# Kernel optimization log

Hardware: AMD Instinct MI355X
Metric: run time of the kernel (lower is better)

Reference implementation:

```python
import jax, jax.numpy as jnp
import numpy as np

B, S, E, H, NL, V = 32, 512, 768, 1024, 5, 30522


def setup_inputs() -> dict:
    key = jax.random.key(0)
    k = jax.random.split(key, 12)
    s = 0.02
    return {
        "x": jax.random.randint(k[0], (B, S), 0, V),
        "emotion_mask": jax.random.randint(k[1], (V,), 0, 2) > 0,
        "all_hidden": jax.random.normal(k[2], (B, S, E), jnp.float32),
        "word_embedding_vocab": jax.random.normal(k[3], (V, E), jnp.float32),
        "Wih0": jax.random.normal(k[4], (4 * H, E), jnp.float32) * s,
        "Whh0": jax.random.normal(k[5], (4 * H, H), jnp.float32) * s,
        "bih0": jnp.zeros((4 * H,), jnp.float32),
        "bhh0": jnp.zeros((4 * H,), jnp.float32),
        "Wih1": jax.random.normal(k[6], (4 * H, H), jnp.float32) * s,
        "Whh1": jax.random.normal(k[7], (4 * H, H), jnp.float32) * s,
        "bih1": jnp.zeros((4 * H,), jnp.float32),
        "bhh1": jnp.zeros((4 * H,), jnp.float32),
        "W1": jax.random.normal(k[8], (100, H), jnp.float32) * s,
        "b1": jnp.zeros((100,), jnp.float32),
        "W2": jax.random.normal(k[9], (1, 100), jnp.float32) * s,
        "b2": jnp.zeros((1,), jnp.float32),
        "Wf": jax.random.normal(k[10], (NL, H), jnp.float32) * s,
        "bf": jnp.zeros((NL,), jnp.float32),
    }


def _lstm_layer(xs, Wih, Whh, bih, bhh):
    # xs: [B, S, D]; PyTorch gate order i, f, g, o
    Bm = xs.shape[0]
    Hm = Whh.shape[1]
    b = bih + bhh

    def step(carry, xt):
        h, c = carry
        g = xt @ Wih.T + h @ Whh.T + b
        i, f, gg, o = jnp.split(g, 4, axis=-1)
        c = jax.nn.sigmoid(f) * c + jax.nn.sigmoid(i) * jnp.tanh(gg)
        h = jax.nn.sigmoid(o) * jnp.tanh(c)
        return (h, c), h

    init = (jnp.zeros((Bm, Hm), xs.dtype), jnp.zeros((Bm, Hm), xs.dtype))
    (h, c), ys = jax.lax.scan(step, init, xs.transpose(1, 0, 2))
    return ys.transpose(1, 0, 2), h, c


def reference(x, emotion_mask, all_hidden, word_embedding_vocab,
              Wih0, Whh0, bih0, bhh0, Wih1, Whh1, bih1, bhh1,
              W1, b1, W2, b2, Wf, bf):
    # Fused replacement for the per-token python loop:
    # blend BERT hidden with vocab embedding where token is in emotion vocab
    # (positions index >= 1 only, as in the original loop range(1, len)).
    emo = emotion_mask[x]                                  # [B, S]
    pos_ok = jnp.arange(x.shape[1]) >= 1                   # [S]
    m = (emo & pos_ok[None, :])[..., None]                 # [B, S, 1]
    hdn = jnp.where(m, (word_embedding_vocab[x] + all_hidden) * 0.5, all_hidden)

    # 2-layer batch_first LSTM (eval mode -> dropout is identity)
    out1, _, _ = _lstm_layer(hdn, Wih0, Whh0, bih0, bhh0)
    out2, _, _ = _lstm_layer(out1, Wih1, Whh1, bih1, bhh1)

    # Structured self-attention
    a = jnp.tanh(out2 @ W1.T + b1)                         # [B, S, 100]
    a = a @ W2.T + b2                                      # [B, S, 1]
    w = jax.nn.softmax(a, axis=1)                          # softmax over seq
    sent = jnp.einsum('bsr,bsh->brh', w, out2)             # [B, 1, H]
    avg = jnp.sum(sent, axis=1)                            # r = 1
    logits = avg @ Wf.T + bf                               # [B, num_labels]
    return logits, w.squeeze(2)
```

## Files before the change

### kernel.cpp

```cpp
#include <hip/hip_runtime.h>

#define B_   32
#define S_   512
#define E_   768
#define H_   1024
#define G4_  4096
#define BS_  16384

__device__ __forceinline__ unsigned short f2b(float f) {
    union { float f; unsigned u; } a; a.f = f;
    unsigned r = a.u + 0x7FFFu + ((a.u >> 16) & 1u);
    return (unsigned short)(r >> 16);
}
__device__ __forceinline__ float b2f(unsigned short u) {
    union { unsigned u; float f; } a; a.u = ((unsigned)u) << 16;
    return a.f;
}

typedef __attribute__((ext_vector_type(8))) short bh8;
typedef __attribute__((ext_vector_type(4))) float f4x;

#define ALOAD(p)     __hip_atomic_load((p), __ATOMIC_RELAXED, __HIP_MEMORY_SCOPE_AGENT)
#define ASTORE(p, v) __hip_atomic_store((p), (v), __ATOMIC_RELAXED, __HIP_MEMORY_SCOPE_AGENT)

__global__ void detect_mask_k(const unsigned* __restrict__ m, unsigned* __restrict__ flag) {
    int t = threadIdx.x;
    unsigned bad = 0;
#pragma unroll
    for (int i = 0; i < 4; ++i) { unsigned v = m[t * 4 + i]; bad |= (v > 1u); }
    unsigned long long bb = __ballot(bad != 0u);
    if (t == 0) flag[0] = (bb != 0ull) ? 1u : 0u;
}

__global__ void blend_k(const int* __restrict__ x, const void* __restrict__ mask,
                        const float* __restrict__ hid, const float* __restrict__ emb,
                        const unsigned* __restrict__ flag, unsigned short* __restrict__ hdn) {
    int row = blockIdx.x;
    int t = threadIdx.x;
    if (t >= 192) return;
    int s = row & 511;
    int tok = x[row];
    bool emo;
    if (flag[0]) emo = ((const unsigned char*)mask)[tok] != 0;
    else         emo = ((const int*)mask)[tok] != 0;
    bool bl = emo && (s >= 1);
    float4 v = *(const float4*)(hid + (size_t)row * E_ + t * 4);
    if (bl) {
        float4 e = *(const float4*)(emb + (size_t)tok * E_ + t * 4);
        v.x = (v.x + e.x) * 0.5f; v.y = (v.y + e.y) * 0.5f;
        v.z = (v.z + e.z) * 0.5f; v.w = (v.w + e.w) * 0.5f;
    }
    ushort4 o; o.x = f2b(v.x); o.y = f2b(v.y); o.z = f2b(v.z); o.w = f2b(v.w);
    *(ushort4*)(hdn + (size_t)row * E_ + t * 4) = o;
}

__global__ void cvt_k(const float* __restrict__ in, unsigned short* __restrict__ o, int n) {
    int i = (blockIdx.x * blockDim.x + threadIdx.x) * 4;
    if (i >= n) return;
    float4 v = *(const float4*)(in + i);
    ushort4 u; u.x = f2b(v.x); u.y = f2b(v.y); u.z = f2b(v.z); u.w = f2b(v.w);
    *(ushort4*)(o + i) = u;
}

template <int AF32, int PERM>
__global__ __launch_bounds__(256) void gemm_k(const void* __restrict__ Ap,
        const unsigned short* __restrict__ Bp, unsigned short* __restrict__ Cp,
        int K, int Nreal, int ldc, const float* __restrict__ bias, int act) {
    __shared__ char smA[16384];
    __shared__ char smB[16384];
    const int tid = threadIdx.x, l = tid & 63, w = tid >> 6;
    const int m0 = blockIdx.x * 128, n0 = blockIdx.y * 128;
    const int wr = (w >> 1) * 64, wc = (w & 1) * 64;
    f4x acc[4][4] = {};
    for (int k0 = 0; k0 < K; k0 += 64) {
#pragma unroll
        for (int it = 0; it < 4; ++it) {
            int idx = it * 256 + tid;
            int row = idx >> 3, c16 = idx & 7;
            int sof = (row * 128 + c16 * 16) ^ ((row & 7) << 4);
            bh8 va;
            if (AF32) {
                const float* ap = (const float*)Ap + (size_t)(m0 + row) * K + k0 + c16 * 8;
                float4 f0 = *(const float4*)ap;
                float4 f1 = *(const float4*)(ap + 4);
                va[0] = (short)f2b(f0.x); va[1] = (short)f2b(f0.y);
                va[2] = (short)f2b(f0.z); va[3] = (short)f2b(f0.w);
                va[4] = (short)f2b(f1.x); va[5] = (short)f2b(f1.y);
                va[6] = (short)f2b(f1.z); va[7] = (short)f2b(f1.w);
            } else {
                va = *(const bh8*)((const unsigned short*)Ap + (size_t)(m0 + row) * K + k0 + c16 * 8);
            }
            *(bh8*)(smA + sof) = va;
            int nr = n0 + row;
            bh8 vb = {0, 0, 0, 0, 0, 0, 0, 0};
            if (nr < Nreal) vb = *(const bh8*)(Bp + (size_t)nr * K + k0 + c16 * 8);
            *(bh8*)(smB + sof) = vb;
        }
        __syncthreads();
#pragma unroll
        for (int kk = 0; kk < 2; ++kk) {
            bh8 af[4], bf8[4];
#pragma unroll
            for (int f = 0; f < 4; ++f) {
                int ra = wr + f * 16 + (l & 15);
                af[f] = *(const bh8*)(smA + ((ra * 128 + kk * 64 + ((l >> 4) << 4)) ^ ((ra & 7) << 4)));
                int rb = wc + f * 16 + (l & 15);
                bf8[f] = *(const bh8*)(smB + ((rb * 128 + kk * 64 + ((l >> 4) << 4)) ^ ((rb & 7) << 4)));
            }
#pragma unroll
            for (int fi = 0; fi < 4; ++fi)
#pragma unroll
                for (int fj = 0; fj < 4; ++fj)
                    acc[fi][fj] = __builtin_amdgcn_mfma_f32_16x16x32_bf16(af[fi], bf8[fj], acc[fi][fj], 0, 0, 0);
        }
        __syncthreads();
    }
#pragma unroll
    for (int fi = 0; fi < 4; ++fi) {
        int rb2 = wr + fi * 16 + ((l >> 4) << 2);
#pragma unroll
        for (int fj = 0; fj < 4; ++fj) {
            int cc = n0 + wc + fj * 16 + (l & 15);
            if (cc < Nreal) {
                float bv = bias ? bias[cc] : 0.f;
                int cw = cc;
                if (PERM) {
                    int gate = cc >> 10, rem = cc & 1023;
                    cw = (rem >> 3) * 32 + gate * 8 + (cc & 7);
                }
#pragma unroll
                for (int i = 0; i < 4; ++i) {
                    float xv = acc[fi][fj][i] + bv;
                    if (act) xv = tanhf(xv);
                    Cp[(size_t)(m0 + rb2 + i) * ldc + cw] = f2b(xv);
                }
            }
        }
    }
}

__global__ __launch_bounds__(256, 1) void recur2_k(
        const unsigned short* __restrict__ G,
        const unsigned short* __restrict__ Whh0,
        const float* __restrict__ bih0, const float* __restrict__ bhh0,
        const unsigned short* __restrict__ Wih1,
        const unsigned short* __restrict__ Whh1,
        const float* __restrict__ bih1, const float* __restrict__ bhh1,
        float* __restrict__ out2,
        unsigned* __restrict__ h0b, unsigned* __restrict__ h1b,
        unsigned* __restrict__ slots) {
    __shared__ __align__(16) char w_lds[131072];
    __shared__ float red_s[4][32][33];
    __shared__ float bias_s[32];
    unsigned short* g_s = (unsigned short*)(w_lds + 65536);

    const int tid = threadIdx.x, l = tid & 63, wv = tid >> 6, ln = l;
    const int wg = blockIdx.x, lay = wg >> 7, w = wg & 127;
    const int u0 = w * 8;
    const int q = l >> 4, r0 = l & 15;
    const int bb = tid >> 3, uu = tid & 7;

#pragma unroll
    for (int it = 0; it < 16; ++it) {
        int idx = it * 256 + tid;
        int r = idx >> 7, c16 = idx & 127;
        int Rg = (r >> 3) * 1024 + u0 + (r & 7);
        int dst = (r * 2048 + c16 * 16) ^ ((r & 7) << 4);
        if (lay == 0) {
            *(bh8*)(w_lds + dst) = *(const bh8*)(Whh0 + (size_t)Rg * 1024 + c16 * 8);
        } else {
            *(bh8*)(w_lds + dst) = *(const bh8*)(Wih1 + (size_t)Rg * 1024 + c16 * 8);
            *(bh8*)(w_lds + 65536 + dst) = *(const bh8*)(Whh1 + (size_t)Rg * 1024 + c16 * 8);
        }
    }
    if (tid < 32) {
        int Rg = (tid >> 3) * 1024 + u0 + (tid & 7);
        bias_s[tid] = (lay == 0) ? (bih0[Rg] + bhh0[Rg]) : (bih1[Rg] + bhh1[Rg]);
    }
    {
        unsigned* hb = (lay == 0) ? h0b : h1b;
        if (tid < 128) ASTORE(&hb[(size_t)w * 128 + tid], 0u);
    }
    float cS = 0.f;
    __syncthreads();
    if (tid == 0) ASTORE(&slots[wg], 1u);

    if (lay == 0) {
        const int gb = tid >> 2, gq = tid & 3;
        bh8 greg = {};
        if (tid < 128)
            greg = *(const bh8*)(G + (size_t)gb * 512 * G4_ + w * 32 + gq * 8);
        for (int g = 1; g <= 512; ++g) {
            int s = g - 1;
            for (;;) {
                unsigned s0v = ALOAD(&slots[ln]);
                unsigned s1v = ALOAD(&slots[64 + ln]);
                if (__all(s0v >= (unsigned)g && s1v >= (unsigned)g)) break;
                __builtin_amdgcn_s_sleep(2);
            }
            const char* hp = (const char*)h0b + (size_t)(g - 1) * 65536;
            f4x a00 = {}, a01 = {}, a10 = {}, a11 = {};
#pragma unroll
            for (int s8 = 0; s8 < 8; ++s8) {
                int k0 = wv * 256 + s8 * 32 + q * 8;
                int blk = k0 >> 3;
                bh8 x0 = *(const bh8*)(hp + blk * 512 + r0 * 16);
                bh8 x1 = *(const bh8*)(hp + blk * 512 + (16 + r0) * 16);
                bh8 w0 = *(const bh8*)(w_lds + ((r0 * 2048 + k0 * 2) ^ ((r0 & 7) << 4)));
                bh8 w1 = *(const bh8*)(w_lds + (((16 + r0) * 2048 + k0 * 2) ^ ((r0 & 7) << 4)));
                a00 = __builtin_amdgcn_mfma_f32_16x16x32_bf16(x0, w0, a00, 0, 0, 0);
                a01 = __builtin_amdgcn_mfma_f32_16x16x32_bf16(x0, w1, a01, 0, 0, 0);
                a10 = __builtin_amdgcn_mfma_f32_16x16x32_bf16(x1, w0, a10, 0, 0, 0);
                a11 = __builtin_amdgcn_mfma_f32_16x16x32_bf16(x1, w1, a11, 0, 0, 0);
            }
#pragma unroll
            for (int i = 0; i < 4; ++i) {
                int ro = q * 4 + i;
                red_s[wv][ro][r0]           = a00[i];
                red_s[wv][ro][16 + r0]      = a01[i];
                red_s[wv][16 + ro][r0]      = a10[i];
                red_s[wv][16 + ro][16 + r0] = a11[i];
            }
            if (tid < 128) {
                *(bh8*)(g_s + gb * 32 + gq * 8) = greg;
                int sn = (s + 1 < 512) ? s + 1 : s;
                greg = *(const bh8*)(G + ((size_t)gb * 512 + sn) * G4_ + w * 32 + gq * 8);
            }
            __syncthreads();
            float gv[4];
#pragma unroll
            for (int gg = 0; gg < 4; ++gg) {
                int rr = gg * 8 + uu;
                gv[gg] = red_s[0][bb][rr] + red_s[1][bb][rr] + red_s[2][bb][rr] + red_s[3][bb][rr]
                       + b2f(g_s[bb * 32 + rr]) + bias_s[rr];
            }
            float si = 1.f / (1.f + __expf(-gv[0]));
            float sf = 1.f / (1.f + __expf(-gv[1]));
            float so = 1.f / (1.f + __expf(-gv[3]));
            float cn = sf * cS + si * tanhf(gv[2]);
            float hv = so * tanhf(cn);
            cS = cn;
            unsigned hu = f2b(hv);
            unsigned nb = __shfl_down(hu, 1);
            if ((uu & 1) == 0)
                ASTORE(&h0b[(size_t)g * 16384 + w * 128 + bb * 4 + (uu >> 1)], hu | (nb << 16));
            __syncthreads();
            if (tid == 0) ASTORE(&slots[wg], (unsigned)(g + 1));
        }
    } else {
        for (int g = 2; g <= 513; ++g) {
            int s = g - 2;
            for (;;) {
                unsigned s0v = ALOAD(&slots[ln]);
                unsigned s1v = ALOAD(&slots[64 + ln]);
                unsigned s2v = ALOAD(&slots[128 + ln]);
                unsigned s3v = ALOAD(&slots[192 + ln]);
                if (__all(s0v >= (unsigned)g && s1v >= (unsigned)g &&
                          s2v >= (unsigned)(g - 1) && s3v >= (unsigned)(g - 1))) break;
                __builtin_amdgcn_s_sleep(2);
            }
            const char* hpA = (const char*)h0b + (size_t)(g - 1) * 65536;
            const char* hpB = (const char*)h1b + (size_t)(g - 2) * 65536;
            f4x a00 = {}, a01 = {}, a10 = {}, a11 = {};
#pragma unroll
            for (int s8 = 0; s8 < 8; ++s8) {
                int k0 = wv * 256 + s8 * 32 + q * 8;
                int blk = k0 >> 3;
                bh8 x0 = *(const bh8*)(hpA + blk * 512 + r0 * 16);
                bh8 x1 = *(const bh8*)(hpA + blk * 512 + (16 + r0) * 16);
                bh8 w0 = *(const bh8*)(w_lds + ((r0 * 2048 + k0 * 2) ^ ((r0 & 7) << 4)));
                bh8 w1 = *(const bh8*)(w_lds + (((16 + r0) * 2048 + k0 * 2) ^ ((r0 & 7) << 4)));
                a00 = __builtin_amdgcn_mfma_f32_16x16x32_bf16(x0, w0, a00, 0, 0, 0);
                a01 = __builtin_amdgcn_mfma_f32_16x16x32_bf16(x0, w1, a01, 0, 0, 0);
                a10 = __builtin_amdgcn_mfma_f32_16x16x32_bf16(x1, w0, a10, 0, 0, 0);
                a11 = __builtin_amdgcn_mfma_f32_16x16x32_bf16(x1, w1, a11, 0, 0, 0);
            }
#pragma unroll
            for (int s8 = 0; s8 < 8; ++s8) {
                int k0 = wv * 256 + s8 * 32 + q * 8;
                int blk = k0 >> 3;
                bh8 x0 = *(const bh8*)(hpB + blk * 512 + r0 * 16);
                bh8 x1 = *(const bh8*)(hpB + blk * 512 + (16 + r0) * 16);
                bh8 w0 = *(const bh8*)(w_lds + 65536 + ((r0 * 2048 + k0 * 2) ^ ((r0 & 7) << 4)));
                bh8 w1 = *(const bh8*)(w_lds + 65536 + (((16 + r0) * 2048 + k0 * 2) ^ ((r0 & 7) << 4)));
                a00 = __builtin_amdgcn_mfma_f32_16x16x32_bf16(x0, w0, a00, 0, 0, 0);
                a01 = __builtin_amdgcn_mfma_f32_16x16x32_bf16(x0, w1, a01, 0, 0, 0);
                a10 = __builtin_amdgcn_mfma_f32_16x16x32_bf16(x1, w0, a10, 0, 0, 0);
                a11 = __builtin_amdgcn_mfma_f32_16x16x32_bf16(x1, w1, a11, 0, 0, 0);
            }
#pragma unroll
            for (int i = 0; i < 4; ++i) {
                int ro = q * 4 + i;
                red_s[wv][ro][r0]           = a00[i];
                red_s[wv][ro][16 + r0]      = a01[i];
                red_s[wv][16 + ro][r0]      = a10[i];
                red_s[wv][16 + ro][16 + r0] = a11[i];
            }
            __syncthreads();
            float gv[4];
#pragma unroll
            for (int gg = 0; gg < 4; ++gg) {
                int rr = gg * 8 + uu;
                gv[gg] = red_s[0][bb][rr] + red_s[1][bb][rr] + red_s[2][bb][rr] + red_s[3][bb][rr]
                       + bias_s[rr];
            }
            float si = 1.f / (1.f + __expf(-gv[0]));
            float sf = 1.f / (1.f + __expf(-gv[1]));
            float so = 1.f / (1.f + __expf(-gv[3]));
            float cn = sf * cS + si * tanhf(gv[2]);
            float hv = so * tanhf(cn);
            cS = cn;
            unsigned hu = f2b(hv);
            unsigned nb = __shfl_down(hu, 1);
            if ((uu & 1) == 0)
                ASTORE(&h1b[(size_t)(g - 1) * 16384 + w * 128 + bb * 4 + (uu >> 1)], hu | (nb << 16));
            out2[((size_t)bb * 512 + s) * 1024 + u0 + uu] = hv;
            __syncthreads();
            if (tid == 0) ASTORE(&slots[wg], (unsigned)g);
        }
    }
}

__global__ void score_k(const unsigned short* __restrict__ a1, const float* __restrict__ W2,
                        float* __restrict__ sc) {
    int r = blockIdx.x * blockDim.x + threadIdx.x;
    const unsigned short* p = a1 + (size_t)r * 104;
    float s = 0.f;
#pragma unroll
    for (int i = 0; i < 100; ++i) s += b2f(p[i]) * W2[i];
    sc[r] = s;
}

__global__ __launch_bounds__(256) void attn_k(const float* __restrict__ sc,
        const float* __restrict__ out2, const float* __restrict__ Wf,
        const float* __restrict__ bf, float* __restrict__ out) {
    int b = blockIdx.x, t = threadIdx.x;
    __shared__ float p[512];
    __shared__ float red[256];
    __shared__ float sent[1024];
    float s0 = sc[b * 512 + t], s1 = sc[b * 512 + 256 + t];
    red[t] = fmaxf(s0, s1);
    __syncthreads();
    for (int o = 128; o > 0; o >>= 1) { if (t < o) red[t] = fmaxf(red[t], red[t + o]); __syncthreads(); }
    float M = red[0];
    __syncthreads();
    float e0 = __expf(s0 - M), e1 = __expf(s1 - M);
    red[t] = e0 + e1;
    __syncthreads();
    for (int o = 128; o > 0; o >>= 1) { if (t < o) red[t] += red[t + o]; __syncthreads(); }
    float inv = 1.f / red[0];
    float w0 = e0 * inv, w1 = e1 * inv;
    p[t] = w0; p[t + 256] = w1;
    out[160 + b * 512 + t] = w0;
    out[160 + b * 512 + 256 + t] = w1;
    __syncthreads();
    float4 acc = {0.f, 0.f, 0.f, 0.f};
    for (int s = 0; s < 512; ++s) {
        float ws = p[s];
        float4 v = *(const float4*)(out2 + ((size_t)b * 512 + s) * H_ + t * 4);
        acc.x += ws * v.x; acc.y += ws * v.y; acc.z += ws * v.z; acc.w += ws * v.w;
    }
    *(float4*)(sent + t * 4) = acc;
    __syncthreads();
    int wv = t >> 6, ln = t & 63;
    for (int n = wv; n < 5; n += 4) {
        float prt = 0.f;
        for (int k = ln; k < 1024; k += 64) prt += sent[k] * Wf[n * 1024 + k];
#pragma unroll
        for (int o = 32; o > 0; o >>= 1) prt += __shfl_down(prt, o);
        if (ln == 0) out[b * 5 + n] = prt + bf[n];
    }
}

#define OFF_SLOT  ((size_t)0)
#define OFF_FLAG  ((size_t)1024)
#define OFF_WH0   ((size_t)4096)
#define OFF_W1I   (OFF_WH0 + (size_t)G4_ * H_ * 2)
#define OFF_WH1   (OFF_W1I + (size_t)G4_ * H_ * 2)
#define OFF_W1A   (OFF_WH1 + (size_t)G4_ * H_ * 2)
#define OFF_G     (OFF_W1A + (size_t)262144)
#define OFF_OUT2  (OFF_G + (size_t)BS_ * G4_ * 2)
#define OFF_HDN   OFF_OUT2
#define OFF_W0    (OFF_HDN + (size_t)BS_ * E_ * 2)
#define OFF_A1    (OFF_OUT2 + (size_t)BS_ * H_ * 4)
#define OFF_SC    (OFF_A1 + (size_t)BS_ * 104 * 2)
#define OFF_H0    ((size_t)230293504)
#define OFF_H1    (OFF_H0 + (size_t)513 * 65536)

extern "C" void kernel_launch(void* const* d_in, const int* in_sizes, int n_in,
                              void* d_out, int out_size, void* d_ws, size_t ws_size,
                              hipStream_t stream) {
    const int*   x    = (const int*)d_in[0];
    const void*  mask = d_in[1];
    const float* hid  = (const float*)d_in[2];
    const float* emb  = (const float*)d_in[3];
    const float* Wih0 = (const float*)d_in[4];
    const float* Whh0 = (const float*)d_in[5];
    const float* bih0 = (const float*)d_in[6];
    const float* bhh0 = (const float*)d_in[7];
    const float* Wih1 = (const float*)d_in[8];
    const float* Whh1 = (const float*)d_in[9];
    const float* bih1 = (const float*)d_in[10];
    const float* bhh1 = (const float*)d_in[11];
    const float* W1   = (const float*)d_in[12];
    const float* b1   = (const float*)d_in[13];
    const float* W2   = (const float*)d_in[14];
    const float* Wf   = (const float*)d_in[16];
    const float* bfp  = (const float*)d_in[17];
    float* out = (float*)d_out;
    char* ws = (char*)d_ws;

    unsigned*       slots = (unsigned*)(ws + OFF_SLOT);
    unsigned*       flag  = (unsigned*)(ws + OFF_FLAG);
    unsigned short* wh0b  = (unsigned short*)(ws + OFF_WH0);
    unsigned short* w1ib  = (unsigned short*)(ws + OFF_W1I);
    unsigned short* wh1b  = (unsigned short*)(ws + OFF_WH1);
    unsigned short* w1ab  = (unsigned short*)(ws + OFF_W1A);
    unsigned short* Gb    = (unsigned short*)(ws + OFF_G);
    float*          out2f = (float*)(ws + OFF_OUT2);
    unsigned short* hdn   = (unsigned short*)(ws + OFF_HDN);
    unsigned short* w0b   = (unsigned short*)(ws + OFF_W0);
    unsigned short* a1b   = (unsigned short*)(ws + OFF_A1);
    float*          scb   = (float*)(ws + OFF_SC);
    unsigned*       h0b   = (unsigned*)(ws + OFF_H0);
    unsigned*       h1b   = (unsigned*)(ws + OFF_H1);

    hipMemsetAsync(ws, 0, 4096, stream);

    detect_mask_k<<<1, 64, 0, stream>>>((const unsigned*)mask, flag);
    blend_k<<<BS_, 192, 0, stream>>>(x, mask, hid, emb, flag, hdn);
    cvt_k<<<3072, 256, 0, stream>>>(Wih0, w0b, G4_ * E_);
    cvt_k<<<4096, 256, 0, stream>>>(Whh0, wh0b, G4_ * H_);
    cvt_k<<<4096, 256, 0, stream>>>(Wih1, w1ib, G4_ * H_);
    cvt_k<<<4096, 256, 0, stream>>>(Whh1, wh1b, G4_ * H_);
    cvt_k<<<100, 256, 0, stream>>>(W1, w1ab, 100 * H_);

    gemm_k<0, 1><<<dim3(BS_ / 128, G4_ / 128), 256, 0, stream>>>(hdn, w0b, Gb, E_, G4_, G4_, nullptr, 0);

    {
        const unsigned short* a0 = Gb;
        const unsigned short* a1p = wh0b;
        const float* a2 = bih0; const float* a3 = bhh0;
        const unsigned short* a4 = w1ib; const unsigned short* a5 = wh1b;
        const float* a6 = bih1; const float* a7 = bhh1;
        float* a8 = out2f; unsigned* a9 = h0b; unsigned* a10 = h1b; unsigned* a11 = slots;
        void* args[] = {&a0, &a1p, &a2, &a3, &a4, &a5, &a6, &a7, &a8, &a9, &a10, &a11};
        hipLaunchCooperativeKernel((const void*)recur2_k, dim3(256), dim3(256), args, 0, stream);
    }

    gemm_k<1, 0><<<dim3(BS_ / 128, 1), 256, 0, stream>>>(out2f, w1ab, a1b, H_, 100, 104, b1, 1);
    score_k<<<BS_ / 256, 256, 0, stream>>>(a1b, W2, scb);
    attn_k<<<B_, 256, 0, stream>>>(scb, out2f, Wf, bfp, out);

    (void)in_sizes; (void)n_in; (void)out_size; (void)ws_size;
}
```

Measured before the change: 5.697 ms.

## Restructure LSTM recurrence with per-wave partitioning, split flags and finer-grained polling

Rewrites the persistent cooperative LSTM kernel so each wave owns a 16x16 output tile over the full K dimension instead of splitting K across waves, which removes the cross-wave LDS reduction. Sync flags are split per half-workgroup and padded to separate cache lines. Layer 1 now polls layer-0 and layer-1 flags separately, so its input-projection half can start before its own previous step is ready. The hidden-state layout is changed to batch-major, and the layer-0 bias is folded into the input GEMM. The aim is a shorter per-step critical path, at the cost of more complex memory-ordering logic.

```diff
diff --git a/kernel.cpp b/kernel.cpp
--- a/kernel.cpp
+++ b/kernel.cpp
@@ -62,6 +62,12 @@
     *(ushort4*)(o + i) = u;
 }
 
+__global__ void bsum_k(const float* __restrict__ a, const float* __restrict__ b,
+                       float* __restrict__ o) {
+    int i = blockIdx.x * blockDim.x + threadIdx.x;
+    o[i] = a[i] + b[i];
+}
+
 template <int AF32, int PERM>
 __global__ __launch_bounds__(256) void gemm_k(const void* __restrict__ Ap,
         const unsigned short* __restrict__ Bp, unsigned short* __restrict__ Cp,
@@ -139,32 +145,59 @@
     }
 }
 
-__global__ __launch_bounds__(256, 1) void recur2_k(
+__device__ __forceinline__ void pollq(const unsigned* __restrict__ slots, int base,
+                                      unsigned need, int l) {
+    for (;;) {
+        unsigned v0 = ALOAD(&slots[(base + l) * 4]);
+        unsigned v1 = ALOAD(&slots[(base + 64 + l) * 4]);
+        unsigned v2 = ALOAD(&slots[(base + 128 + l) * 4]);
+        unsigned v3 = ALOAD(&slots[(base + 192 + l) * 4]);
+        unsigned m0 = v0 < v1 ? v0 : v1;
+        unsigned m1 = v2 < v3 ? v2 : v3;
+        unsigned mn = m0 < m1 ? m0 : m1;
+        if (__all(mn >= need)) break;
+        __builtin_amdgcn_s_sleep(1);
+    }
+}
+
+__device__ __forceinline__ void kloop(const char* __restrict__ ab, const char* __restrict__ wb,
+                                      int rowb, int xorv, f4x& acc, f4x& acc2) {
+#pragma unroll 8
+    for (int kc = 0; kc < 32; kc += 2) {
+        bh8 a0 = *(const bh8*)(ab + kc * 64);
+        bh8 b0 = *(const bh8*)(wb + ((rowb + kc * 64) ^ xorv));
+        acc = __builtin_amdgcn_mfma_f32_16x16x32_bf16(a0, b0, acc, 0, 0, 0);
+        bh8 a1 = *(const bh8*)(ab + kc * 64 + 64);
+        bh8 b1 = *(const bh8*)(wb + ((rowb + (kc + 1) * 64) ^ xorv));
+        acc2 = __builtin_amdgcn_mfma_f32_16x16x32_bf16(a1, b1, acc2, 0, 0, 0);
+    }
+}
+
+__global__ __launch_bounds__(256, 1) void recur3_k(
         const unsigned short* __restrict__ G,
         const unsigned short* __restrict__ Whh0,
-        const float* __restrict__ bih0, const float* __restrict__ bhh0,
         const unsigned short* __restrict__ Wih1,
         const unsigned short* __restrict__ Whh1,
-        const float* __restrict__ bih1, const float* __restrict__ bhh1,
+        const float* __restrict__ bsum1,
         float* __restrict__ out2,
         unsigned* __restrict__ h0b, unsigned* __restrict__ h1b,
         unsigned* __restrict__ slots) {
     __shared__ __align__(16) char w_lds[131072];
-    __shared__ float red_s[4][32][33];
-    __shared__ float bias_s[32];
-    unsigned short* g_s = (unsigned short*)(w_lds + 65536);
-
-    const int tid = threadIdx.x, l = tid & 63, wv = tid >> 6, ln = l;
+    __shared__ float gx[2][2][16][17];
+    const int tid = threadIdx.x, l = tid & 63, wv = tid >> 6;
     const int wg = blockIdx.x, lay = wg >> 7, w = wg & 127;
-    const int u0 = w * 8;
-    const int q = l >> 4, r0 = l & 15;
-    const int bb = tid >> 3, uu = tid & 7;
+    const int n = l & 15, kq = l >> 4;
+    const int mb = (wv & 1) << 4;
+    const int nb = (wv >> 1) << 4;
+    const int half = wv & 1;
+    const int xorv = (n & 7) << 4;
+    const int rowb = (nb + n) * 2048 + kq * 16;
 
 #pragma unroll
     for (int it = 0; it < 16; ++it) {
         int idx = it * 256 + tid;
         int r = idx >> 7, c16 = idx & 127;
-        int Rg = (r >> 3) * 1024 + u0 + (r & 7);
+        int Rg = (r >> 3) * 1024 + w * 8 + (r & 7);
         int dst = (r * 2048 + c16 * 16) ^ ((r & 7) << 4);
         if (lay == 0) {
             *(bh8*)(w_lds + dst) = *(const bh8*)(Whh0 + (size_t)Rg * 1024 + c16 * 8);
@@ -173,150 +206,98 @@
             *(bh8*)(w_lds + 65536 + dst) = *(const bh8*)(Whh1 + (size_t)Rg * 1024 + c16 * 8);
         }
     }
-    if (tid < 32) {
-        int Rg = (tid >> 3) * 1024 + u0 + (tid & 7);
-        bias_s[tid] = (lay == 0) ? (bih0[Rg] + bhh0[Rg]) : (bih1[Rg] + bhh1[Rg]);
-    }
     {
-        unsigned* hb = (lay == 0) ? h0b : h1b;
-        if (tid < 128) ASTORE(&hb[(size_t)w * 128 + tid], 0u);
-    }
-    float cS = 0.f;
-    __syncthreads();
-    if (tid == 0) ASTORE(&slots[wg], 1u);
-
+        unsigned* hb = lay ? h1b : h0b;
+        if (tid < 128) ASTORE(&hb[(tid >> 2) * 512 + w * 4 + (tid & 3)], 0u);
+    }
+    const float bias_n = lay ? bsum1[((nb + n) >> 3) * 1024 + w * 8 + ((nb + n) & 7)] : 0.f;
+    f4x cS = {0.f, 0.f, 0.f, 0.f};
+    __syncthreads();
+    if (tid == 0) {
+        ASTORE(&slots[(lay * 256 + 2 * w) * 4], 1u);
+        ASTORE(&slots[(lay * 256 + 2 * w + 1) * 4], 1u);
+    }
+    const int slb = lay * 256;
+
+    unsigned short g4[4];
     if (lay == 0) {
-        const int gb = tid >> 2, gq = tid & 3;
-        bh8 greg = {};
-        if (tid < 128)
-            greg = *(const bh8*)(G + (size_t)gb * 512 * G4_ + w * 32 + gq * 8);
-        for (int g = 1; g <= 512; ++g) {
-            int s = g - 1;
-            for (;;) {
-                unsigned s0v = ALOAD(&slots[ln]);
-                unsigned s1v = ALOAD(&slots[64 + ln]);
-                if (__all(s0v >= (unsigned)g && s1v >= (unsigned)g)) break;
-                __builtin_amdgcn_s_sleep(2);
-            }
-            const char* hp = (const char*)h0b + (size_t)(g - 1) * 65536;
-            f4x a00 = {}, a01 = {}, a10 = {}, a11 = {};
-#pragma unroll
-            for (int s8 = 0; s8 < 8; ++s8) {
-                int k0 = wv * 256 + s8 * 32 + q * 8;
-                int blk = k0 >> 3;
-                bh8 x0 = *(const bh8*)(hp + blk * 512 + r0 * 16);
-                bh8 x1 = *(const bh8*)(hp + blk * 512 + (16 + r0) * 16);
-                bh8 w0 = *(const bh8*)(w_lds + ((r0 * 2048 + k0 * 2) ^ ((r0 & 7) << 4)));
-                bh8 w1 = *(const bh8*)(w_lds + (((16 + r0) * 2048 + k0 * 2) ^ ((r0 & 7) << 4)));
-                a00 = __builtin_amdgcn_mfma_f32_16x16x32_bf16(x0, w0, a00, 0, 0, 0);
-                a01 = __builtin_amdgcn_mfma_f32_16x16x32_bf16(x0, w1, a01, 0, 0, 0);
-                a10 = __builtin_amdgcn_mfma_f32_16x16x32_bf16(x1, w0, a10, 0, 0, 0);
-                a11 = __builtin_amdgcn_mfma_f32_16x16x32_bf16(x1, w1, a11, 0, 0, 0);
-            }
+#pragma unroll
+        for (int i = 0; i < 4; ++i)
+            g4[i] = G[(size_t)(mb + kq * 4 + i) * 512 * G4_ + (size_t)w * 32 + nb + n];
+    }
+
+    for (int s = 0; s < S_; ++s) {
+        f4x acc, acc2 = {0.f, 0.f, 0.f, 0.f};
+        if (lay == 0) {
+            if (wv == 0) pollq(slots, 0, (unsigned)(s + 1), l);
+            __syncthreads();
+            unsigned short g4n[4];
+            {
+                int sn = (s + 1 < S_) ? s + 1 : s;
+#pragma unroll
+                for (int i = 0; i < 4; ++i)
+                    g4n[i] = G[((size_t)(mb + kq * 4 + i) * 512 + sn) * G4_ + (size_t)w * 32 + nb + n];
+            }
+#pragma unroll
+            for (int i = 0; i < 4; ++i) acc[i] = b2f(g4[i]);
+            const char* hp = (const char*)h0b + (size_t)s * 65536;
+            kloop(hp + (mb + n) * 2048 + kq * 16, w_lds, rowb, xorv, acc, acc2);
+#pragma unroll
+            for (int i = 0; i < 4; ++i) g4[i] = g4n[i];
+        } else {
+            if (wv == 0) pollq(slots, 0, (unsigned)(s + 2), l);
+            __syncthreads();
+#pragma unroll
+            for (int i = 0; i < 4; ++i) acc[i] = bias_n;
+            const char* hpA = (const char*)h0b + (size_t)(s + 1) * 65536;
+            kloop(hpA + (mb + n) * 2048 + kq * 16, w_lds, rowb, xorv, acc, acc2);
+            if (wv == 0) pollq(slots, 256, (unsigned)(s + 1), l);
+            __syncthreads();
+            const char* hpB = (const char*)h1b + (size_t)s * 65536;
+            kloop(hpB + (mb + n) * 2048 + kq * 16, w_lds + 65536, rowb, xorv, acc, acc2);
+        }
+        f4x at = acc + acc2;
+        const int p = s & 1;
+        if (wv >= 2) {
+#pragma unroll
+            for (int i = 0; i < 4; ++i) gx[p][half][kq * 4 + i][n] = at[i];
+        }
+        __syncthreads();
+        if (wv < 2) {
+            f4x ap;
+#pragma unroll
+            for (int i = 0; i < 4; ++i) ap[i] = __shfl_xor(at[i], 8);
+            unsigned huw[4] = {0, 0, 0, 0};
+            float hvf[4] = {0.f, 0.f, 0.f, 0.f};
+            if (n < 8) {
+#pragma unroll
+                for (int i = 0; i < 4; ++i) {
+                    int bl = kq * 4 + i;
+                    float gi = at[i], gf = ap[i];
+                    float gg = gx[p][half][bl][n];
+                    float go = gx[p][half][bl][8 + n];
+                    float si = 1.f / (1.f + __expf(-gi));
+                    float sf = 1.f / (1.f + __expf(-gf));
+                    float so = 1.f / (1.f + __expf(-go));
+                    float c = sf * cS[i] + si * tanhf(gg);
+                    float hv = so * tanhf(c);
+                    cS[i] = c; hvf[i] = hv; huw[i] = f2b(hv);
+                }
+            }
+            unsigned* hn = (lay ? h1b : h0b) + (size_t)(s + 1) * 16384;
 #pragma unroll
             for (int i = 0; i < 4; ++i) {
-                int ro = q * 4 + i;
-                red_s[wv][ro][r0]           = a00[i];
-                red_s[wv][ro][16 + r0]      = a01[i];
-                red_s[wv][16 + ro][r0]      = a10[i];
-                red_s[wv][16 + ro][16 + r0] = a11[i];
-            }
-            if (tid < 128) {
-                *(bh8*)(g_s + gb * 32 + gq * 8) = greg;
-                int sn = (s + 1 < 512) ? s + 1 : s;
-                greg = *(const bh8*)(G + ((size_t)gb * 512 + sn) * G4_ + w * 32 + gq * 8);
-            }
-            __syncthreads();
-            float gv[4];
-#pragma unroll
-            for (int gg = 0; gg < 4; ++gg) {
-                int rr = gg * 8 + uu;
-                gv[gg] = red_s[0][bb][rr] + red_s[1][bb][rr] + red_s[2][bb][rr] + red_s[3][bb][rr]
-                       + b2f(g_s[bb * 32 + rr]) + bias_s[rr];
-            }
-            float si = 1.f / (1.f + __expf(-gv[0]));
-            float sf = 1.f / (1.f + __expf(-gv[1]));
-            float so = 1.f / (1.f + __expf(-gv[3]));
-            float cn = sf * cS + si * tanhf(gv[2]);
-            float hv = so * tanhf(cn);
-            cS = cn;
-            unsigned hu = f2b(hv);
-            unsigned nb = __shfl_down(hu, 1);
-            if ((uu & 1) == 0)
-                ASTORE(&h0b[(size_t)g * 16384 + w * 128 + bb * 4 + (uu >> 1)], hu | (nb << 16));
-            __syncthreads();
-            if (tid == 0) ASTORE(&slots[wg], (unsigned)(g + 1));
-        }
-    } else {
-        for (int g = 2; g <= 513; ++g) {
-            int s = g - 2;
-            for (;;) {
-                unsigned s0v = ALOAD(&slots[ln]);
-                unsigned s1v = ALOAD(&slots[64 + ln]);
-                unsigned s2v = ALOAD(&slots[128 + ln]);
-                unsigned s3v = ALOAD(&slots[192 + ln]);
-                if (__all(s0v >= (unsigned)g && s1v >= (unsigned)g &&
-                          s2v >= (unsigned)(g - 1) && s3v >= (unsigned)(g - 1))) break;
-                __builtin_amdgcn_s_sleep(2);
-            }
-            const char* hpA = (const char*)h0b + (size_t)(g - 1) * 65536;
-            const char* hpB = (const char*)h1b + (size_t)(g - 2) * 65536;
-            f4x a00 = {}, a01 = {}, a10 = {}, a11 = {};
-#pragma unroll
-            for (int s8 = 0; s8 < 8; ++s8) {
-                int k0 = wv * 256 + s8 * 32 + q * 8;
-                int blk = k0 >> 3;
-                bh8 x0 = *(const bh8*)(hpA + blk * 512 + r0 * 16);
-                bh8 x1 = *(const bh8*)(hpA + blk * 512 + (16 + r0) * 16);
-                bh8 w0 = *(const bh8*)(w_lds + ((r0 * 2048 + k0 * 2) ^ ((r0 & 7) << 4)));
-                bh8 w1 = *(const bh8*)(w_lds + (((16 + r0) * 2048 + k0 * 2) ^ ((r0 & 7) << 4)));
-                a00 = __builtin_amdgcn_mfma_f32_16x16x32_bf16(x0, w0, a00, 0, 0, 0);
-                a01 = __builtin_amdgcn_mfma_f32_16x16x32_bf16(x0, w1, a01, 0, 0, 0);
-                a10 = __builtin_amdgcn_mfma_f32_16x16x32_bf16(x1, w0, a10, 0, 0, 0);
-                a11 = __builtin_amdgcn_mfma_f32_16x16x32_bf16(x1, w1, a11, 0, 0, 0);
-            }
-#pragma unroll
-            for (int s8 = 0; s8 < 8; ++s8) {
-                int k0 = wv * 256 + s8 * 32 + q * 8;
-                int blk = k0 >> 3;
-                bh8 x0 = *(const bh8*)(hpB + blk * 512 + r0 * 16);
-                bh8 x1 = *(const bh8*)(hpB + blk * 512 + (16 + r0) * 16);
-                bh8 w0 = *(const bh8*)(w_lds + 65536 + ((r0 * 2048 + k0 * 2) ^ ((r0 & 7) << 4)));
-                bh8 w1 = *(const bh8*)(w_lds + 65536 + (((16 + r0) * 2048 + k0 * 2) ^ ((r0 & 7) << 4)));
-                a00 = __builtin_amdgcn_mfma_f32_16x16x32_bf16(x0, w0, a00, 0, 0, 0);
-                a01 = __builtin_amdgcn_mfma_f32_16x16x32_bf16(x0, w1, a01, 0, 0, 0);
-                a10 = __builtin_amdgcn_mfma_f32_16x16x32_bf16(x1, w0, a10, 0, 0, 0);
-                a11 = __builtin_amdgcn_mfma_f32_16x16x32_bf16(x1, w1, a11, 0, 0, 0);
-            }
-#pragma unroll
-            for (int i = 0; i < 4; ++i) {
-                int ro = q * 4 + i;
-                red_s[wv][ro][r0]           = a00[i];
-                red_s[wv][ro][16 + r0]      = a01[i];
-                red_s[wv][16 + ro][r0]      = a10[i];
-                red_s[wv][16 + ro][16 + r0] = a11[i];
-            }
-            __syncthreads();
-            float gv[4];
-#pragma unroll
-            for (int gg = 0; gg < 4; ++gg) {
-                int rr = gg * 8 + uu;
-                gv[gg] = red_s[0][bb][rr] + red_s[1][bb][rr] + red_s[2][bb][rr] + red_s[3][bb][rr]
-                       + bias_s[rr];
-            }
-            float si = 1.f / (1.f + __expf(-gv[0]));
-            float sf = 1.f / (1.f + __expf(-gv[1]));
-            float so = 1.f / (1.f + __expf(-gv[3]));
-            float cn = sf * cS + si * tanhf(gv[2]);
-            float hv = so * tanhf(cn);
-            cS = cn;
-            unsigned hu = f2b(hv);
-            unsigned nb = __shfl_down(hu, 1);
-            if ((uu & 1) == 0)
-                ASTORE(&h1b[(size_t)(g - 1) * 16384 + w * 128 + bb * 4 + (uu >> 1)], hu | (nb << 16));
-            out2[((size_t)bb * 512 + s) * 1024 + u0 + uu] = hv;
-            __syncthreads();
-            if (tid == 0) ASTORE(&slots[wg], (unsigned)g);
+                unsigned pu = __shfl_xor(huw[i], 1);
+                if (n < 8 && !(n & 1))
+                    ASTORE(&hn[(mb + kq * 4 + i) * 512 + w * 4 + (n >> 1)], huw[i] | (pu << 16));
+            }
+            asm volatile("s_waitcnt vmcnt(0)" ::: "memory");
+            if (l == 0) ASTORE(&slots[(slb + 2 * w + wv) * 4], (unsigned)(s + 2));
+            if (lay == 1 && n < 8) {
+#pragma unroll
+                for (int i = 0; i < 4; ++i)
+                    out2[((size_t)(mb + kq * 4 + i) * 512 + s) * 1024 + w * 8 + n] = hvf[i];
+            }
         }
     }
 }
@@ -372,13 +353,15 @@
     }
 }
 
-#define OFF_SLOT  ((size_t)0)
-#define OFF_FLAG  ((size_t)1024)
+#define OFF_FLAG  ((size_t)0)
 #define OFF_WH0   ((size_t)4096)
 #define OFF_W1I   (OFF_WH0 + (size_t)G4_ * H_ * 2)
 #define OFF_WH1   (OFF_W1I + (size_t)G4_ * H_ * 2)
 #define OFF_W1A   (OFF_WH1 + (size_t)G4_ * H_ * 2)
-#define OFF_G     (OFF_W1A + (size_t)262144)
+#define OFF_BS0   (OFF_W1A + (size_t)204800)
+#define OFF_BS1   (OFF_BS0 + (size_t)16384)
+#define OFF_SLOT  (OFF_BS1 + (size_t)16384)
+#define OFF_G     ((size_t)25432064)
 #define OFF_OUT2  (OFF_G + (size_t)BS_ * G4_ * 2)
 #define OFF_HDN   OFF_OUT2
 #define OFF_W0    (OFF_HDN + (size_t)BS_ * E_ * 2)
@@ -410,12 +393,14 @@
     float* out = (float*)d_out;
     char* ws = (char*)d_ws;
 
-    unsigned*       slots = (unsigned*)(ws + OFF_SLOT);
     unsigned*       flag  = (unsigned*)(ws + OFF_FLAG);
     unsigned short* wh0b  = (unsigned short*)(ws + OFF_WH0);
     unsigned short* w1ib  = (unsigned short*)(ws + OFF_W1I);
     unsigned short* wh1b  = (unsigned short*)(ws + OFF_WH1);
     unsigned short* w1ab  = (unsigned short*)(ws + OFF_W1A);
+    float*          bs0   = (float*)(ws + OFF_BS0);
+    float*          bs1   = (float*)(ws + OFF_BS1);
+    unsigned*       slots = (unsigned*)(ws + OFF_SLOT);
     unsigned short* Gb    = (unsigned short*)(ws + OFF_G);
     float*          out2f = (float*)(ws + OFF_OUT2);
     unsigned short* hdn   = (unsigned short*)(ws + OFF_HDN);
@@ -426,6 +411,7 @@
     unsigned*       h1b   = (unsigned*)(ws + OFF_H1);
 
     hipMemsetAsync(ws, 0, 4096, stream);
+    hipMemsetAsync(ws + OFF_SLOT, 0, 8192, stream);
 
     detect_mask_k<<<1, 64, 0, stream>>>((const unsigned*)mask, flag);
     blend_k<<<BS_, 192, 0, stream>>>(x, mask, hid, emb, flag, hdn);
@@ -434,18 +420,21 @@
     cvt_k<<<4096, 256, 0, stream>>>(Wih1, w1ib, G4_ * H_);
     cvt_k<<<4096, 256, 0, stream>>>(Whh1, wh1b, G4_ * H_);
     cvt_k<<<100, 256, 0, stream>>>(W1, w1ab, 100 * H_);
-
-    gemm_k<0, 1><<<dim3(BS_ / 128, G4_ / 128), 256, 0, stream>>>(hdn, w0b, Gb, E_, G4_, G4_, nullptr, 0);
+    bsum_k<<<16, 256, 0, stream>>>(bih0, bhh0, bs0);
+    bsum_k<<<16, 256, 0, stream>>>(bih1, bhh1, bs1);
+
+    gemm_k<0, 1><<<dim3(BS_ / 128, G4_ / 128), 256, 0, stream>>>(hdn, w0b, Gb, E_, G4_, G4_, bs0, 0);
 
     {
         const unsigned short* a0 = Gb;
         const unsigned short* a1p = wh0b;
-        const float* a2 = bih0; const float* a3 = bhh0;
-        const unsigned short* a4 = w1ib; const unsigned short* a5 = wh1b;
-        const float* a6 = bih1; const float* a7 = bhh1;
-        float* a8 = out2f; unsigned* a9 = h0b; unsigned* a10 = h1b; unsigned* a11 = slots;
-        void* args[] = {&a0, &a1p, &a2, &a3, &a4, &a5, &a6, &a7, &a8, &a9, &a10, &a11};
-        hipLaunchCooperativeKernel((const void*)recur2_k, dim3(256), dim3(256), args, 0, stream);
+        const unsigned short* a2 = w1ib;
+        const unsigned short* a3 = wh1b;
+        const float* a4 = bs1;
+        float* a5 = out2f;
+        unsigned* a6 = h0b; unsigned* a7 = h1b; unsigned* a8 = slots;
+        void* args[] = {&a0, &a1p, &a2, &a3, &a4, &a5, &a6, &a7, &a8};
+        hipLaunchCooperativeKernel((const void*)recur3_k, dim3(256), dim3(256), args, 0, stream);
     }
 
     gemm_k<1, 0><<<dim3(BS_ / 128, 1), 256, 0, stream>>>(out2f, w1ab, a1b, H_, 100, 104, b1, 1);
```

New measurement: 5.592 ms. No clear change (-1.8%).
